# Optimization experiments

Measured on AMD Instinct MI355X. Metric: run time of the kernel, lower is better.

Reference implementation:

```python
import jax, jax.numpy as jnp
import numpy as np

B, T, C, F = 2, 2048, 2048, 8192
LN_EPS = 1e-5


def setup_inputs() -> dict:
    key = jax.random.key(0)
    ks = jax.random.split(key, 24)
    rn = lambda k, s, sc=1.0: jax.random.normal(k, s, jnp.float32) * sc
    un = lambda k, s: jax.random.uniform(k, s, jnp.float32)
    inp = {}
    inp['x'] = rn(ks[0], (B, T, C))
    inp['att_shift'] = rn(ks[1], (B, C))
    # wkv_state rows: aa (num), bb (den), pp (running max exponent)
    inp['wkv_state'] = jnp.stack([jnp.zeros((B, C)), jnp.zeros((B, C)),
                                  jnp.full((B, C), -1e38)], axis=1)
    inp['ffn_shift'] = rn(ks[2], (B, C))
    inp['ln1_g'] = jnp.ones(C); inp['ln1_b'] = jnp.zeros(C)
    inp['ln2_g'] = jnp.ones(C); inp['ln2_b'] = jnp.zeros(C)
    inp['tmk'] = un(ks[3], (C,)); inp['tmv'] = un(ks[4], (C,)); inp['tmr'] = un(ks[5], (C,))
    inp['time_decay'] = rn(ks[6], (C,), 0.5)
    inp['time_first'] = rn(ks[7], (C,), 0.5)
    inp['Wk'] = rn(ks[8], (C, C), 0.02); inp['Wv'] = rn(ks[9], (C, C), 0.02)
    inp['Wr'] = rn(ks[10], (C, C), 0.02); inp['Wo'] = rn(ks[11], (C, C), 0.02)
    inp['fmk'] = un(ks[12], (C,)); inp['fmr'] = un(ks[13], (C,))
    inp['Fk'] = rn(ks[14], (C, F), 0.02)
    inp['Fr'] = rn(ks[15], (C, C), 0.02)
    inp['Fv'] = rn(ks[16], (F, C), 0.02)
    return inp


def layer_norm(x, g, b):
    m = jnp.mean(x, axis=-1, keepdims=True)
    v = jnp.mean(jnp.square(x - m), axis=-1, keepdims=True)
    return (x - m) * jax.lax.rsqrt(v + LN_EPS) * g + b


def wkv(w, u, k, v, state):
    # w: -exp(time_decay) [C], u: time_first [C]; k,v: [B,T,C]; state: [B,3,C]
    def step(carry, kv_t):
        aa, bb, pp = carry
        kt, vt = kv_t
        ww = u + kt
        p = jnp.maximum(pp, ww)
        e1 = jnp.exp(pp - p)
        e2 = jnp.exp(ww - p)
        y = (e1 * aa + e2 * vt) / (e1 * bb + e2)
        ww2 = pp + w
        p2 = jnp.maximum(ww2, kt)
        e1b = jnp.exp(ww2 - p2)
        e2b = jnp.exp(kt - p2)
        return (e1b * aa + e2b * vt, e1b * bb + e2b, p2), y
    carry0 = (state[:, 0], state[:, 1], state[:, 2])
    (aa, bb, pp), ys = jax.lax.scan(step, carry0,
                                    (k.transpose(1, 0, 2), v.transpose(1, 0, 2)))
    return ys.transpose(1, 0, 2), jnp.stack([aa, bb, pp], axis=1)


def reference(x, att_shift, wkv_state, ffn_shift, ln1_g, ln1_b, ln2_g, ln2_b,
              tmk, tmv, tmr, time_decay, time_first, Wk, Wv, Wr, Wo,
              fmk, fmr, Fk, Fr, Fv):
    # ---- time-mix (attention) ----
    x1 = layer_norm(x, ln1_g, ln1_b)
    xx = jnp.concatenate([att_shift[:, None, :], x1[:, :-1]], axis=1)
    xk = x1 * tmk + xx * (1.0 - tmk)
    xv = x1 * tmv + xx * (1.0 - tmv)
    xr = x1 * tmr + xx * (1.0 - tmr)
    k = jnp.einsum('btc,cd->btd', xk, Wk)
    v = jnp.einsum('btc,cd->btd', xv, Wv)
    r = jnp.einsum('btc,cd->btd', xr, Wr)
    y, new_wkv = wkv(-jnp.exp(time_decay), time_first, k, v, wkv_state)
    x = x + jnp.einsum('btd,dc->btc', jax.nn.sigmoid(r) * y, Wo)
    # ---- channel-mix (FFN) ----
    x2 = layer_norm(x, ln2_g, ln2_b)
    xx2 = jnp.concatenate([ffn_shift[:, None, :], x2[:, :-1]], axis=1)
    xk2 = x2 * fmk + xx2 * (1.0 - fmk)
    xr2 = x2 * fmr + xx2 * (1.0 - fmr)
    kf = jnp.square(jax.nn.relu(jnp.einsum('btc,cf->btf', xk2, Fk)))
    kv = jnp.einsum('btf,fc->btc', kf, Fv)
    x = x + jax.nn.sigmoid(jnp.einsum('btc,cd->btd', xr2, Fr)) * kv
    return x, x1[:, -1], new_wkv, x2[:, -1]
```

## Files before the change

kernel.cpp:

```cpp
#include <hip/hip_runtime.h>
#include <stdint.h>

#define B_ 2
#define T_ 2048
#define C_ 2048
#define F_ 8192
#define M_ 4096
#define BC_ 4096
#define CHB 16
#define TCH 16
#define LC2 128

typedef __attribute__((ext_vector_type(8))) __bf16 bf16x8;
typedef __attribute__((ext_vector_type(4))) float f32x4;

__device__ __forceinline__ unsigned short f2bf(float f) {
  union { float f; unsigned u; } v; v.f = f;
  unsigned r = v.u + 0x7fffu + ((v.u >> 16) & 1u);
  return (unsigned short)(r >> 16);
}
__device__ __forceinline__ float b2f(unsigned short h) {
  union { unsigned u; float f; } v; v.u = ((unsigned)h) << 16; return v.f;
}

__device__ __forceinline__ void gload16(const void* g, void* l) {
  __builtin_amdgcn_global_load_lds((__attribute__((address_space(1))) void*)g,
                                   (__attribute__((address_space(3))) void*)l,
                                   16, 0, 0);
}

__device__ __forceinline__ void transpose_tile(
    const float* __restrict__ W, unsigned short* __restrict__ out,
    int K, int N, int k0, int n0) {
  __shared__ unsigned short tile[32][66];
  const int tx = threadIdx.x & 31, ty = threadIdx.x >> 5;
#pragma unroll
  for (int i = 0; i < 8; ++i)
    tile[tx][ty + 8 * i] = f2bf(W[(size_t)(k0 + ty + 8 * i) * N + n0 + tx]);
  __syncthreads();
#pragma unroll
  for (int j = 0; j < 4; ++j) {
    const int nn = ty + 8 * j;
    const unsigned pk = *(const unsigned*)&tile[nn][2 * tx];
    *(unsigned*)&out[(size_t)(n0 + nn) * K + k0 + 2 * tx] = pk;
  }
}

__global__ __launch_bounds__(256) void k_transpose4(
    const float* __restrict__ W0, const float* __restrict__ W1,
    const float* __restrict__ W2, const float* __restrict__ W3,
    unsigned short* __restrict__ WT) {
  const float* W = (blockIdx.z == 0) ? W0 : (blockIdx.z == 1) ? W1
                   : (blockIdx.z == 2) ? W2 : W3;
  unsigned short* out = WT + (size_t)blockIdx.z * C_ * C_;
  transpose_tile(W, out, C_, C_, blockIdx.x * 64, blockIdx.y * 32);
}

__global__ __launch_bounds__(256) void k_transpose1(
    const float* __restrict__ W, unsigned short* __restrict__ WT, int K, int N) {
  transpose_tile(W, WT, K, N, blockIdx.x * 64, blockIdx.y * 32);
}

__global__ __launch_bounds__(256) void k_layernorm(
    const float* __restrict__ x, const float* __restrict__ g,
    const float* __restrict__ beta, unsigned short* __restrict__ y,
    float* __restrict__ last_out) {
  const int row = blockIdx.x;
  const int t = row & (T_ - 1);
  const int bi = row >> 11;
  const float* xr = x + (size_t)row * C_;
  const int base = threadIdx.x * 8;
  float lv[8];
  {
    float4 a = *(const float4*)(xr + base);
    float4 b = *(const float4*)(xr + base + 4);
    lv[0]=a.x; lv[1]=a.y; lv[2]=a.z; lv[3]=a.w; lv[4]=b.x; lv[5]=b.y; lv[6]=b.z; lv[7]=b.w;
  }
  float s = 0.f, q = 0.f;
#pragma unroll
  for (int j = 0; j < 8; ++j) { s += lv[j]; q += lv[j] * lv[j]; }
#pragma unroll
  for (int o = 32; o > 0; o >>= 1) { s += __shfl_down(s, o); q += __shfl_down(q, o); }
  __shared__ float rs[4], rq[4];
  if ((threadIdx.x & 63) == 0) { rs[threadIdx.x >> 6] = s; rq[threadIdx.x >> 6] = q; }
  __syncthreads();
  s = rs[0] + rs[1] + rs[2] + rs[3];
  q = rq[0] + rq[1] + rq[2] + rq[3];
  const float mean = s * (1.f / C_);
  const float var = q * (1.f / C_) - mean * mean;
  const float inv = 1.f / sqrtf(var + 1e-5f);
  float ov[8];
  unsigned short o8[8];
#pragma unroll
  for (int j = 0; j < 8; ++j) {
    ov[j] = (lv[j] - mean) * inv * g[base + j] + beta[base + j];
    o8[j] = f2bf(ov[j]);
  }
  *(uint4*)(y + (size_t)row * C_ + base) = *(uint4*)o8;
  if (last_out != nullptr && t == T_ - 1) {
    float* lp = last_out + (size_t)bi * C_ + base;
    *(float4*)lp = make_float4(ov[0], ov[1], ov[2], ov[3]);
    *(float4*)(lp + 4) = make_float4(ov[4], ov[5], ov[6], ov[7]);
  }
}

__global__ __launch_bounds__(256) void k_mix3(
    const unsigned short* __restrict__ x1, const float* __restrict__ shift,
    const float* __restrict__ tmk, const float* __restrict__ tmv,
    const float* __restrict__ tmr,
    unsigned short* __restrict__ xk, unsigned short* __restrict__ xv,
    unsigned short* __restrict__ xr) {
  const int row = blockIdx.x;
  const int t = row & (T_ - 1);
  const int bi = row >> 11;
  const int c0 = threadIdx.x * 8;
  const size_t o = (size_t)row * C_ + c0;
  unsigned short cur8[8];
  *(uint4*)cur8 = *(const uint4*)(x1 + o);
  float pv[8];
  if (t == 0) {
    const float* sp = shift + (size_t)bi * C_ + c0;
#pragma unroll
    for (int j = 0; j < 8; ++j) pv[j] = sp[j];
  } else {
    unsigned short p8[8];
    *(uint4*)p8 = *(const uint4*)(x1 + o - C_);
#pragma unroll
    for (int j = 0; j < 8; ++j) pv[j] = b2f(p8[j]);
  }
  unsigned short ok[8], ov[8], orr[8];
#pragma unroll
  for (int j = 0; j < 8; ++j) {
    const float a = b2f(cur8[j]), p = pv[j];
    const float mk = tmk[c0 + j], mv = tmv[c0 + j], mr = tmr[c0 + j];
    ok[j]  = f2bf(a * mk + p * (1.f - mk));
    ov[j]  = f2bf(a * mv + p * (1.f - mv));
    orr[j] = f2bf(a * mr + p * (1.f - mr));
  }
  *(uint4*)(xk + o) = *(uint4*)ok;
  *(uint4*)(xv + o) = *(uint4*)ov;
  *(uint4*)(xr + o) = *(uint4*)orr;
}

__global__ __launch_bounds__(256) void k_mix2(
    const unsigned short* __restrict__ x2, const float* __restrict__ shift,
    const float* __restrict__ fmk, const float* __restrict__ fmr,
    unsigned short* __restrict__ xk2, unsigned short* __restrict__ xr2) {
  const int row = blockIdx.x;
  const int t = row & (T_ - 1);
  const int bi = row >> 11;
  const int c0 = threadIdx.x * 8;
  const size_t o = (size_t)row * C_ + c0;
  unsigned short cur8[8];
  *(uint4*)cur8 = *(const uint4*)(x2 + o);
  float pv[8];
  if (t == 0) {
    const float* sp = shift + (size_t)bi * C_ + c0;
#pragma unroll
    for (int j = 0; j < 8; ++j) pv[j] = sp[j];
  } else {
    unsigned short p8[8];
    *(uint4*)p8 = *(const uint4*)(x2 + o - C_);
#pragma unroll
    for (int j = 0; j < 8; ++j) pv[j] = b2f(p8[j]);
  }
  unsigned short ok[8], orr[8];
#pragma unroll
  for (int j = 0; j < 8; ++j) {
    const float a = b2f(cur8[j]), p = pv[j];
    const float mk = fmk[c0 + j], mr = fmr[c0 + j];
    ok[j]  = f2bf(a * mk + p * (1.f - mk));
    orr[j] = f2bf(a * mr + p * (1.f - mr));
  }
  *(uint4*)(xk2 + o) = *(uint4*)ok;
  *(uint4*)(xr2 + o) = *(uint4*)orr;
}

__global__ __launch_bounds__(256) void k_wkv_sry(
    const float* __restrict__ kk, const float* __restrict__ vv,
    const unsigned short* __restrict__ rr,
    const float* __restrict__ td, const float* __restrict__ tf,
    const float* __restrict__ st, unsigned short* __restrict__ sry,
    float* __restrict__ out_state) {
  __shared__ float sA[TCH][CHB], sB[TCH][CHB], sP[TCH][CHB];
  const int blk = blockIdx.x;
  const int bi = blk >> 7;
  const int tx = threadIdx.x & 15;
  const int ty = threadIdx.x >> 4;
  const int c = ((blk & 127) * CHB) + tx;
  const float w = -expf(td[c]);
  const float u = tf[c];
  const size_t base = (size_t)bi * T_ * C_ + (size_t)ty * LC2 * C_ + c;
  const float* kp = kk + base;
  const float* vp = vv + base;
  float aa = 0.f, bb = 0.f, pp = -1e38f;
#pragma unroll 8
  for (int i = 0; i < LC2; ++i) {
    const float kt = kp[(size_t)i * C_], vt = vp[(size_t)i * C_];
    const float ww2 = pp + w;
    const float p2 = fmaxf(ww2, kt);
    const float e1b = expf(ww2 - p2), e2b = expf(kt - p2);
    aa = e1b * aa + e2b * vt;
    bb = e1b * bb + e2b;
    pp = p2;
  }
  sA[ty][tx] = aa; sB[ty][tx] = bb; sP[ty][tx] = pp;
  __syncthreads();
  if (ty == 0) {
    const float* s0 = st + (size_t)bi * 3 * C_;
    float ca = s0[c], cb = s0[C_ + c], cp = s0[2 * C_ + c];
    const float wL = w * (float)LC2;
#pragma unroll
    for (int j = 0; j < TCH; ++j) {
      const float a2 = sA[j][tx], b2 = sB[j][tx], p2 = sP[j][tx];
      sA[j][tx] = ca; sB[j][tx] = cb; sP[j][tx] = cp;
      const float pd = cp + wL;
      const float pm = fmaxf(pd, p2);
      const float e1 = expf(pd - pm), e2 = expf(p2 - pm);
      ca = e1 * ca + e2 * a2;
      cb = e1 * cb + e2 * b2;
      cp = pm;
    }
  }
  __syncthreads();
  aa = sA[ty][tx]; bb = sB[ty][tx]; pp = sP[ty][tx];
  const unsigned short* rp = rr + base;
  unsigned short* sp2 = sry + base;
#pragma unroll 4
  for (int i = 0; i < LC2; ++i) {
    const float kt = kp[(size_t)i * C_], vt = vp[(size_t)i * C_];
    const float ww = u + kt;
    const float p = fmaxf(pp, ww);
    const float e1 = expf(pp - p), e2 = expf(ww - p);
    const float yv = (e1 * aa + e2 * vt) / (e1 * bb + e2);
    const float rv = b2f(rp[(size_t)i * C_]);
    const float sg = 1.f / (1.f + expf(-rv));
    sp2[(size_t)i * C_] = f2bf(sg * yv);
    const float ww2 = pp + w;
    const float p2 = fmaxf(ww2, kt);
    const float e1b = expf(ww2 - p2), e2b = expf(kt - p2);
    aa = e1b * aa + e2b * vt;
    bb = e1b * bb + e2b;
    pp = p2;
  }
  if (ty == TCH - 1) {
    float* ob = out_state + (size_t)bi * 3 * C_;
    ob[c] = aa; ob[C_ + c] = bb; ob[2 * C_ + c] = pp;
  }
}

template <int EPI, int SWZ>
__global__ __launch_bounds__(512, 1) void k_gemm8(
    const unsigned short* __restrict__ A, const unsigned short* __restrict__ BT,
    int K, int Nn, void* __restrict__ out,
    const float* __restrict__ aux1, const float* __restrict__ aux2) {
  __shared__ unsigned short lds[73728];
  const int tid = threadIdx.x;
  const int lane = tid & 63;
  const int wid = tid >> 6;
  int mBase, nBase;
  if (SWZ) {
    const int gx = gridDim.x, gy = gridDim.y;
    const int wg = blockIdx.y * gx + blockIdx.x;
    const int per = (gx * gy) >> 3;
    const int p = 31 - __clz(per);
    const int nr = 1 << ((p - 1) >> 1);
    const int mr = per / nr;
    if ((gx % nr) == 0 && (gy % mr) == 0) {
      const int gxr = gx / nr;
      const int xcd = wg & 7, idx = wg >> 3;
      const int rr = xcd / gxr, rc = xcd % gxr;
      mBase = (rr * mr + idx / nr) * 128;
      nBase = (rc * nr + idx % nr) * 256;
    } else {
      int w2 = (wg & 7) * per + (wg >> 3);
      mBase = (w2 / gx) * 128;
      nBase = (w2 % gx) * 256;
    }
  } else {
    mBase = blockIdx.y * 128;
    nBase = blockIdx.x * 256;
  }
  const int wr = (wid >> 2) * 64;
  const int wc = (wid & 3) * 64;
  const int r16 = lane & 15, kq = lane >> 4;
  const int lrow = lane >> 3;
  const int lslot = (lane & 7) ^ lrow;
  const int xsw = r16 & 7;
  f32x4 acc[4][4] = {};

  const unsigned short* gA0 = A  + (size_t)(mBase + 0   + wid * 8 + lrow) * K + lslot * 8;
  const unsigned short* gA1 = A  + (size_t)(mBase + 64  + wid * 8 + lrow) * K + lslot * 8;
  const unsigned short* gB0 = BT + (size_t)(nBase + 0   + wid * 8 + lrow) * K + lslot * 8;
  const unsigned short* gB1 = BT + (size_t)(nBase + 64  + wid * 8 + lrow) * K + lslot * 8;
  const unsigned short* gB2 = BT + (size_t)(nBase + 128 + wid * 8 + lrow) * K + lslot * 8;
  const unsigned short* gB3 = BT + (size_t)(nBase + 192 + wid * 8 + lrow) * K + lslot * 8;
  const int wof = wid * 512;
  int aoff[4][2], boff[4][2];
#pragma unroll
  for (int m = 0; m < 4; ++m)
#pragma unroll
    for (int s = 0; s < 2; ++s)
      aoff[m][s] = (wr + m * 16 + r16) * 64 + (((s * 4 + kq) ^ xsw) * 8);
#pragma unroll
  for (int n = 0; n < 4; ++n)
#pragma unroll
    for (int s = 0; s < 2; ++s)
      boff[n][s] = 8192 + (wc + n * 16 + r16) * 64 + (((s * 4 + kq) ^ xsw) * 8);

  const int nt = K >> 6;
  gload16(gA0, &lds[0 + wof]);
  gload16(gA1, &lds[4096 + wof]);
  gload16(gB0, &lds[8192 + wof]);
  gload16(gB1, &lds[12288 + wof]);
  gload16(gB2, &lds[16384 + wof]);
  gload16(gB3, &lds[20480 + wof]);
  gload16(gA0 + 64, &lds[24576 + 0 + wof]);
  gload16(gA1 + 64, &lds[24576 + 4096 + wof]);
  gload16(gB0 + 64, &lds[24576 + 8192 + wof]);
  gload16(gB1 + 64, &lds[24576 + 12288 + wof]);
  gload16(gB2 + 64, &lds[24576 + 16384 + wof]);
  gload16(gB3 + 64, &lds[24576 + 20480 + wof]);
  asm volatile("s_waitcnt vmcnt(6)" ::: "memory");
  asm volatile("s_barrier" ::: "memory");

  int cb = 0;
  for (int t = 0; t < nt; ++t) {
    const int nb = (cb >= 1) ? cb - 1 : 2;
    const int ca = cb * 24576;
    const int nba = nb * 24576;
    const int kb2 = (t + 2) << 6;
    const bool pf = (t + 2) < nt;
    if (pf) {
      gload16(gA0 + kb2, &lds[nba + 0 + wof]);
      gload16(gA1 + kb2, &lds[nba + 4096 + wof]);
      gload16(gB0 + kb2, &lds[nba + 8192 + wof]);
      gload16(gB1 + kb2, &lds[nba + 12288 + wof]);
      gload16(gB2 + kb2, &lds[nba + 16384 + wof]);
      gload16(gB3 + kb2, &lds[nba + 20480 + wof]);
    }
    bf16x8 af[4][2], bq[4][2];
#pragma unroll
    for (int m = 0; m < 4; ++m)
#pragma unroll
      for (int s = 0; s < 2; ++s)
        af[m][s] = *(const bf16x8*)&lds[ca + aoff[m][s]];
#pragma unroll
    for (int n = 0; n < 4; ++n)
#pragma unroll
      for (int s = 0; s < 2; ++s)
        bq[n][s] = *(const bf16x8*)&lds[ca + boff[n][s]];
    __builtin_amdgcn_s_setprio(1);
#pragma unroll
    for (int m = 0; m < 4; ++m)
#pragma unroll
      for (int n = 0; n < 4; ++n)
#pragma unroll
        for (int s = 0; s < 2; ++s)
          acc[m][n] = __builtin_amdgcn_mfma_f32_16x16x32_bf16(
              af[m][s], bq[n][s], acc[m][n], 0, 0, 0);
    __builtin_amdgcn_s_setprio(0);
    if (pf) {
      asm volatile("s_waitcnt vmcnt(6)" ::: "memory");
    } else if (t + 1 < nt) {
      asm volatile("s_waitcnt vmcnt(0)" ::: "memory");
    }
    asm volatile("s_barrier" ::: "memory");
    cb = (cb == 2) ? 0 : cb + 1;
  }

  const int c0 = kq * 4;
#pragma unroll
  for (int m = 0; m < 4; ++m) {
#pragma unroll
    for (int n = 0; n < 4; ++n) {
      const int col = nBase + wc + n * 16 + r16;
#pragma unroll
      for (int e = 0; e < 4; ++e) {
        const int rowg = mBase + wr + m * 16 + c0 + e;
        const size_t idx = (size_t)rowg * Nn + col;
        const float va = acc[m][n][e];
        if (EPI == 0) {
          ((float*)out)[idx] = va;
        } else if (EPI == 1) {
          const float t = va > 0.f ? va : 0.f;
          ((unsigned short*)out)[idx] = f2bf(t * t);
        } else if (EPI == 2) {
          ((float*)out)[idx] = aux1[idx] + va;
        } else if (EPI == 3) {
          const float s = 1.f / (1.f + expf(-va));
          ((float*)out)[idx] = aux1[idx] + s * aux2[idx];
        } else {
          ((unsigned short*)out)[idx] = f2bf(va);
        }
      }
    }
  }
}

template <int EPI, int SWZ>
__global__ __launch_bounds__(512, 1) void k_gemm256(
    const unsigned short* __restrict__ A, const unsigned short* __restrict__ BT,
    int K, int Nn, void* __restrict__ out,
    const float* __restrict__ aux1, const float* __restrict__ aux2) {
  __shared__ unsigned short lds[65536];
  const int tid = threadIdx.x;
  const int lane = tid & 63;
  const int wid = tid >> 6;
  int mBase, nBase;
  if (SWZ) {
    const int gx = gridDim.x, gy = gridDim.y;
    const int wg = blockIdx.y * gx + blockIdx.x;
    const int per = (gx * gy) >> 3;
    const int p = 31 - __clz(per);
    const int nr = 1 << (p >> 1);
    const int mr = per / nr;
    if ((gx % nr) == 0 && (gy % mr) == 0) {
      const int gxr = gx / nr;
      const int xcd = wg & 7, idx = wg >> 3;
      const int rr = xcd / gxr, rc = xcd % gxr;
      mBase = (rr * mr + idx / nr) * 256;
      nBase = (rc * nr + idx % nr) * 256;
    } else {
      int w2 = (wg & 7) * per + (wg >> 3);
      mBase = (w2 / gx) * 256;
      nBase = (w2 % gx) * 256;
    }
  } else {
    mBase = blockIdx.y * 256;
    nBase = blockIdx.x * 256;
  }
  const int wr = (wid >> 2) * 128;
  const int wc = (wid & 3) * 64;
  const int r16 = lane & 15, kq = lane >> 4;
  const int lrow = lane >> 3;
  const int lslot = (lane & 7) ^ lrow;
  const int xsw = r16 & 7;
  f32x4 acc[8][4] = {};

  const unsigned short* gA[4];
  const unsigned short* gB[4];
#pragma unroll
  for (int j = 0; j < 4; ++j) {
    gA[j] = A  + (size_t)(mBase + j * 64 + wid * 8 + lrow) * K + lslot * 8;
    gB[j] = BT + (size_t)(nBase + j * 64 + wid * 8 + lrow) * K + lslot * 8;
  }
  const int wof = wid * 512;

  const int nt = K >> 6;
#pragma unroll
  for (int j = 0; j < 4; ++j) {
    gload16(gA[j], &lds[j * 4096 + wof]);
    gload16(gB[j], &lds[16384 + j * 4096 + wof]);
  }
  asm volatile("s_waitcnt vmcnt(0)" ::: "memory");
  asm volatile("s_barrier" ::: "memory");

  for (int t = 0; t < nt; ++t) {
    const int ca = (t & 1) * 32768;
    const int nba = ((t + 1) & 1) * 32768;
    const int kb1 = (t + 1) << 6;
    const bool pf = (t + 1) < nt;
    if (pf) {
#pragma unroll
      for (int j = 0; j < 4; ++j) {
        gload16(gA[j] + kb1, &lds[nba + j * 4096 + wof]);
        gload16(gB[j] + kb1, &lds[nba + 16384 + j * 4096 + wof]);
      }
    }
    bf16x8 bq[4][2];
#pragma unroll
    for (int n = 0; n < 4; ++n)
#pragma unroll
      for (int s = 0; s < 2; ++s)
        bq[n][s] = *(const bf16x8*)&lds[ca + 16384 + (wc + n * 16 + r16) * 64 +
                                        (((s * 4 + kq) ^ xsw) * 8)];
#pragma unroll
    for (int qm = 0; qm < 2; ++qm) {
      bf16x8 af[4][2];
#pragma unroll
      for (int m = 0; m < 4; ++m)
#pragma unroll
        for (int s = 0; s < 2; ++s)
          af[m][s] = *(const bf16x8*)&lds[ca + (wr + (qm * 4 + m) * 16 + r16) * 64 +
                                          (((s * 4 + kq) ^ xsw) * 8)];
      __builtin_amdgcn_s_setprio(1);
#pragma unroll
      for (int m = 0; m < 4; ++m)
#pragma unroll
        for (int n = 0; n < 4; ++n)
#pragma unroll
          for (int s = 0; s < 2; ++s)
            acc[qm * 4 + m][n] = __builtin_amdgcn_mfma_f32_16x16x32_bf16(
                af[m][s], bq[n][s], acc[qm * 4 + m][n], 0, 0, 0);
      __builtin_amdgcn_s_setprio(0);
    }
    if (pf) asm volatile("s_waitcnt vmcnt(0)" ::: "memory");
    asm volatile("s_barrier" ::: "memory");
  }

  const int c0 = kq * 4;
#pragma unroll
  for (int m = 0; m < 8; ++m) {
#pragma unroll
    for (int n = 0; n < 4; ++n) {
      const int col = nBase + wc + n * 16 + r16;
#pragma unroll
      for (int e = 0; e < 4; ++e) {
        const int rowg = mBase + wr + m * 16 + c0 + e;
        const size_t idx = (size_t)rowg * Nn + col;
        const float va = acc[m][n][e];
        if (EPI == 0) {
          ((float*)out)[idx] = va;
        } else if (EPI == 1) {
          const float t = va > 0.f ? va : 0.f;
          ((unsigned short*)out)[idx] = f2bf(t * t);
        } else if (EPI == 2) {
          ((float*)out)[idx] = aux1[idx] + va;
        } else if (EPI == 3) {
          const float s = 1.f / (1.f + expf(-va));
          ((float*)out)[idx] = aux1[idx] + s * aux2[idx];
        } else {
          ((unsigned short*)out)[idx] = f2bf(va);
        }
      }
    }
  }
}

extern "C" void kernel_launch(void* const* d_in, const int* in_sizes, int n_in,
                              void* d_out, int out_size, void* d_ws, size_t ws_size,
                              hipStream_t stream) {
  const float* x          = (const float*)d_in[0];
  const float* att_shift  = (const float*)d_in[1];
  const float* wkv_state  = (const float*)d_in[2];
  const float* ffn_shift  = (const float*)d_in[3];
  const float* ln1_g = (const float*)d_in[4];
  const float* ln1_b = (const float*)d_in[5];
  const float* ln2_g = (const float*)d_in[6];
  const float* ln2_b = (const float*)d_in[7];
  const float* tmk = (const float*)d_in[8];
  const float* tmv = (const float*)d_in[9];
  const float* tmr = (const float*)d_in[10];
  const float* time_decay = (const float*)d_in[11];
  const float* time_first = (const float*)d_in[12];
  const float* Wk = (const float*)d_in[13];
  const float* Wv = (const float*)d_in[14];
  const float* Wr = (const float*)d_in[15];
  const float* Wo = (const float*)d_in[16];
  const float* fmk = (const float*)d_in[17];
  const float* fmr = (const float*)d_in[18];
  const float* Fk = (const float*)d_in[19];
  const float* Fr = (const float*)d_in[20];
  const float* Fv = (const float*)d_in[21];

  const size_t MB = 1ull << 20;
  char* ws = (char*)d_ws;
  if (ws_size < 176 * MB) return;

  unsigned short* Wslot = (unsigned short*)(ws);
  float*          kBuf  = (float*)(ws + 32 * MB);
  float*          vBuf  = (float*)(ws + 64 * MB);
  float*          yBuf  = (float*)(ws + 96 * MB);
  unsigned short* h1    = (unsigned short*)(ws + 128 * MB);
  unsigned short* h2    = (unsigned short*)(ws + 144 * MB);
  unsigned short* h3    = (unsigned short*)(ws + 160 * MB);
  unsigned short* xrT   = (unsigned short*)kBuf;
  unsigned short* kf    = (unsigned short*)kBuf;
  float*          kv    = (float*)h1;
  unsigned short* sWr = Wslot + 0 * (size_t)C_ * C_;
  unsigned short* sWk = Wslot + 1 * (size_t)C_ * C_;
  unsigned short* sWv = Wslot + 2 * (size_t)C_ * C_;
  unsigned short* sWo = Wslot + 3 * (size_t)C_ * C_;

  float* outb    = (float*)d_out;
  float* x1_last = outb + (size_t)M_ * C_;
  float* wkv_out = x1_last + (size_t)B_ * C_;
  float* x2_last = wkv_out + (size_t)B_ * 3 * C_;

  const dim3 gC8(C_ / 256, M_ / 128);
  const dim3 gF256(F_ / 256, M_ / 256);

  k_transpose4<<<dim3(C_ / 64, C_ / 32, 4), 256, 0, stream>>>(Wr, Wk, Wv, Wo, Wslot);
  k_layernorm<<<M_, 256, 0, stream>>>(x, ln1_g, ln1_b, h1, x1_last);
  k_mix3<<<M_, 256, 0, stream>>>(h1, att_shift, tmk, tmv, tmr, h2, h3, xrT);
  k_gemm8<4,1><<<gC8, 512, 0, stream>>>(xrT, sWr, C_, C_, h1, nullptr, nullptr);
  k_gemm8<0,1><<<gC8, 512, 0, stream>>>(h2, sWk, C_, C_, kBuf, nullptr, nullptr);
  k_gemm8<0,1><<<gC8, 512, 0, stream>>>(h3, sWv, C_, C_, vBuf, nullptr, nullptr);
  k_wkv_sry<<<dim3(BC_ / CHB), 256, 0, stream>>>(kBuf, vBuf, h1, time_decay, time_first,
                                                 wkv_state, h2, wkv_out);
  k_gemm8<2,1><<<gC8, 512, 0, stream>>>(h2, sWo, C_, C_, yBuf, x, nullptr);

  k_layernorm<<<M_, 256, 0, stream>>>(yBuf, ln2_g, ln2_b, h1, x2_last);
  k_mix2<<<M_, 256, 0, stream>>>(h1, ffn_shift, fmk, fmr, h2, h3);
  k_transpose1<<<dim3(C_ / 64, F_ / 32), 256, 0, stream>>>(Fk, Wslot, C_, F_);
  k_gemm256<1,1><<<gF256, 512, 0, stream>>>(h2, Wslot, C_, F_, kf, nullptr, nullptr);
  k_transpose1<<<dim3(F_ / 64, C_ / 32), 256, 0, stream>>>(Fv, Wslot, F_, C_);
  k_gemm8<0,1><<<gC8, 512, 0, stream>>>(kf, Wslot, F_, C_, kv, nullptr, nullptr);
  k_transpose1<<<dim3(C_ / 64, C_ / 32), 256, 0, stream>>>(Fr, Wslot, C_, C_);
  k_gemm8<3,1><<<gC8, 512, 0, stream>>>(h3, Wslot, C_, C_, d_out, yBuf, kv);
}
```

Baseline: 629.4 us.

## Split-K the FFN down-projection on 256x256 tiles with bf16 partials

The K=8192 Fv GEMM moves from the 128x256-tile kernel to the 256x256-tile kernel, split into two K halves along grid z so the block count stays the same. Each half writes a bf16 partial product into separate workspace slices. The final Fr GEMM gets a new epilogue that adds the two partials before the sigmoid gating and residual add. The aim is higher arithmetic intensity per block on the largest-K GEMM. The cost is rounding the partial sums to bf16, which loses precision compared with the previous single fp32 output.

```diff
diff --git a/kernel.cpp b/kernel.cpp
--- a/kernel.cpp
+++ b/kernel.cpp
@@ -253,7 +253,8 @@
 __global__ __launch_bounds__(512, 1) void k_gemm8(
     const unsigned short* __restrict__ A, const unsigned short* __restrict__ BT,
     int K, int Nn, void* __restrict__ out,
-    const float* __restrict__ aux1, const float* __restrict__ aux2) {
+    const float* __restrict__ aux1, const void* __restrict__ aux2,
+    const void* __restrict__ aux3) {
   __shared__ unsigned short lds[73728];
   const int tid = threadIdx.x;
   const int lane = tid & 63;
@@ -389,7 +390,12 @@
           ((float*)out)[idx] = aux1[idx] + va;
         } else if (EPI == 3) {
           const float s = 1.f / (1.f + expf(-va));
-          ((float*)out)[idx] = aux1[idx] + s * aux2[idx];
+          ((float*)out)[idx] = aux1[idx] + s * ((const float*)aux2)[idx];
+        } else if (EPI == 5) {
+          const float s = 1.f / (1.f + expf(-va));
+          const float kvv = b2f(((const unsigned short*)aux2)[idx]) +
+                            b2f(((const unsigned short*)aux3)[idx]);
+          ((float*)out)[idx] = aux1[idx] + s * kvv;
         } else {
           ((unsigned short*)out)[idx] = f2bf(va);
         }
@@ -401,12 +407,13 @@
 template <int EPI, int SWZ>
 __global__ __launch_bounds__(512, 1) void k_gemm256(
     const unsigned short* __restrict__ A, const unsigned short* __restrict__ BT,
-    int K, int Nn, void* __restrict__ out,
-    const float* __restrict__ aux1, const float* __restrict__ aux2) {
+    int K, int Klen, int Nn, void* __restrict__ out, size_t outStride) {
   __shared__ unsigned short lds[65536];
   const int tid = threadIdx.x;
   const int lane = tid & 63;
   const int wid = tid >> 6;
+  const int Koff = blockIdx.z * Klen;
+  void* outz = (char*)out + (size_t)blockIdx.z * outStride;
   int mBase, nBase;
   if (SWZ) {
     const int gx = gridDim.x, gy = gridDim.y;
@@ -442,12 +449,12 @@
   const unsigned short* gB[4];
 #pragma unroll
   for (int j = 0; j < 4; ++j) {
-    gA[j] = A  + (size_t)(mBase + j * 64 + wid * 8 + lrow) * K + lslot * 8;
-    gB[j] = BT + (size_t)(nBase + j * 64 + wid * 8 + lrow) * K + lslot * 8;
+    gA[j] = A  + (size_t)(mBase + j * 64 + wid * 8 + lrow) * K + Koff + lslot * 8;
+    gB[j] = BT + (size_t)(nBase + j * 64 + wid * 8 + lrow) * K + Koff + lslot * 8;
   }
   const int wof = wid * 512;
 
-  const int nt = K >> 6;
+  const int nt = Klen >> 6;
 #pragma unroll
   for (int j = 0; j < 4; ++j) {
     gload16(gA[j], &lds[j * 4096 + wof]);
@@ -511,17 +518,12 @@
         const size_t idx = (size_t)rowg * Nn + col;
         const float va = acc[m][n][e];
         if (EPI == 0) {
-          ((float*)out)[idx] = va;
+          ((float*)outz)[idx] = va;
         } else if (EPI == 1) {
           const float t = va > 0.f ? va : 0.f;
-          ((unsigned short*)out)[idx] = f2bf(t * t);
-        } else if (EPI == 2) {
-          ((float*)out)[idx] = aux1[idx] + va;
-        } else if (EPI == 3) {
-          const float s = 1.f / (1.f + expf(-va));
-          ((float*)out)[idx] = aux1[idx] + s * aux2[idx];
+          ((unsigned short*)outz)[idx] = f2bf(t * t);
         } else {
-          ((unsigned short*)out)[idx] = f2bf(va);
+          ((unsigned short*)outz)[idx] = f2bf(va);
         }
       }
     }
@@ -567,7 +569,7 @@
   unsigned short* h3    = (unsigned short*)(ws + 160 * MB);
   unsigned short* xrT   = (unsigned short*)kBuf;
   unsigned short* kf    = (unsigned short*)kBuf;
-  float*          kv    = (float*)h1;
+  unsigned short* kvp   = (unsigned short*)h1;
   unsigned short* sWr = Wslot + 0 * (size_t)C_ * C_;
   unsigned short* sWk = Wslot + 1 * (size_t)C_ * C_;
   unsigned short* sWv = Wslot + 2 * (size_t)C_ * C_;
@@ -580,23 +582,25 @@
 
   const dim3 gC8(C_ / 256, M_ / 128);
   const dim3 gF256(F_ / 256, M_ / 256);
+  const dim3 gKV(C_ / 256, M_ / 256, 2);
 
   k_transpose4<<<dim3(C_ / 64, C_ / 32, 4), 256, 0, stream>>>(Wr, Wk, Wv, Wo, Wslot);
   k_layernorm<<<M_, 256, 0, stream>>>(x, ln1_g, ln1_b, h1, x1_last);
   k_mix3<<<M_, 256, 0, stream>>>(h1, att_shift, tmk, tmv, tmr, h2, h3, xrT);
-  k_gemm8<4,1><<<gC8, 512, 0, stream>>>(xrT, sWr, C_, C_, h1, nullptr, nullptr);
-  k_gemm8<0,1><<<gC8, 512, 0, stream>>>(h2, sWk, C_, C_, kBuf, nullptr, nullptr);
-  k_gemm8<0,1><<<gC8, 512, 0, stream>>>(h3, sWv, C_, C_, vBuf, nullptr, nullptr);
+  k_gemm8<4,1><<<gC8, 512, 0, stream>>>(xrT, sWr, C_, C_, h1, nullptr, nullptr, nullptr);
+  k_gemm8<0,1><<<gC8, 512, 0, stream>>>(h2, sWk, C_, C_, kBuf, nullptr, nullptr, nullptr);
+  k_gemm8<0,1><<<gC8, 512, 0, stream>>>(h3, sWv, C_, C_, vBuf, nullptr, nullptr, nullptr);
   k_wkv_sry<<<dim3(BC_ / CHB), 256, 0, stream>>>(kBuf, vBuf, h1, time_decay, time_first,
                                                  wkv_state, h2, wkv_out);
-  k_gemm8<2,1><<<gC8, 512, 0, stream>>>(h2, sWo, C_, C_, yBuf, x, nullptr);
+  k_gemm8<2,1><<<gC8, 512, 0, stream>>>(h2, sWo, C_, C_, yBuf, x, nullptr, nullptr);
 
   k_layernorm<<<M_, 256, 0, stream>>>(yBuf, ln2_g, ln2_b, h1, x2_last);
   k_mix2<<<M_, 256, 0, stream>>>(h1, ffn_shift, fmk, fmr, h2, h3);
   k_transpose1<<<dim3(C_ / 64, F_ / 32), 256, 0, stream>>>(Fk, Wslot, C_, F_);
-  k_gemm256<1,1><<<gF256, 512, 0, stream>>>(h2, Wslot, C_, F_, kf, nullptr, nullptr);
+  k_gemm256<1,1><<<gF256, 512, 0, stream>>>(h2, Wslot, C_, C_, F_, kf, 0);
   k_transpose1<<<dim3(F_ / 64, C_ / 32), 256, 0, stream>>>(Fv, Wslot, F_, C_);
-  k_gemm8<0,1><<<gC8, 512, 0, stream>>>(kf, Wslot, F_, C_, kv, nullptr, nullptr);
+  k_gemm256<4,1><<<gKV, 512, 0, stream>>>(kf, Wslot, F_, F_ / 2, C_, kvp, 16 * MB);
   k_transpose1<<<dim3(C_ / 64, C_ / 32), 256, 0, stream>>>(Fr, Wslot, C_, C_);
-  k_gemm8<3,1><<<gC8, 512, 0, stream>>>(h3, Wslot, C_, C_, d_out, yBuf, kv);
-}
+  k_gemm8<5,1><<<gC8, 512, 0, stream>>>(h3, Wslot, C_, C_, d_out, yBuf,
+                                        kvp, kvp + 8 * (size_t)MB);
+}
```

After: 618.0 us. No clear change (-1.8%).
